# Optimization experiments

Measured on AMD Instinct MI355X. Metric: run time of the kernel, lower is better.

Reference implementation:

```python
import jax, jax.numpy as jnp
import numpy as np

PHM_DIM = 4
IN_FEATS = 2048
OUT_FEATS = 8192
TOKENS = 8192


def setup_inputs() -> dict:
    key = jax.random.key(0)
    k_x, k_rule, k_w = jax.random.split(key, 3)
    x = jax.random.normal(k_x, (TOKENS, IN_FEATS), dtype=jnp.float32)
    # c_init='normal', std=0.01
    phm_rule = 0.01 * jax.random.normal(k_rule, (PHM_DIM, PHM_DIM, PHM_DIM), dtype=jnp.float32)
    # w_init='normal', std=phm_init_range=1e-4 (scaled up here for numerics of the test)
    W = 1e-4 * jax.random.normal(k_w, (PHM_DIM, IN_FEATS // PHM_DIM, OUT_FEATS // PHM_DIM), dtype=jnp.float32)
    b = jnp.zeros((OUT_FEATS,), dtype=jnp.float32)
    return {"x": x, "phm_rule": phm_rule, "W": W, "b": b}


def reference(x, phm_rule, W, b):
    # H = sum_i kron(phm_rule[i], W[i])  with shape (phm_dim*in_per, phm_dim*out_per)
    # kron(A, B)[a*in_per + c, k*out_per + p] = A[a, k] * B[c, p]
    d, in_per, out_per = W.shape
    H = jnp.einsum('iak,icp->acKp'.replace('K', 'k'), phm_rule, W)  # (d, in_per, d, out_per)
    H = H.reshape(d * in_per, d * out_per)
    y = x @ H + b
    return y
```

## Files before the change

kernel.cpp:

```cpp
#include <hip/hip_runtime.h>
#include <stdint.h>

#define PHM      4
#define IN_FEATS 2048
#define OUT_FEATS 8192
#define TOKENS   8192
#define IN_PER   512
#define OUT_PER  2048

typedef __attribute__((ext_vector_type(8)))  short short8;
typedef __attribute__((ext_vector_type(16))) float f32x16;
typedef __attribute__((ext_vector_type(8)))  unsigned short u16x8;

__device__ inline unsigned short f2bf(float f) {
    unsigned int u = __builtin_bit_cast(unsigned int, f);
    u += 0x7fffu + ((u >> 16) & 1u);
    return (unsigned short)(u >> 16);
}

__global__ void cvt_x_kernel(const float* __restrict__ x,
                             unsigned short* __restrict__ xb) {
    int i = blockIdx.x * blockDim.x + threadIdx.x;
    const float4* x4 = (const float4*)x;
    float4 v0 = x4[2 * i];
    float4 v1 = x4[2 * i + 1];
    u16x8 o;
    o[0] = f2bf(v0.x); o[1] = f2bf(v0.y); o[2] = f2bf(v0.z); o[3] = f2bf(v0.w);
    o[4] = f2bf(v1.x); o[5] = f2bf(v1.y); o[6] = f2bf(v1.z); o[7] = f2bf(v1.w);
    *(u16x8*)(xb + 8 * (size_t)i) = o;
}

__global__ void build_ht_kernel(const float* __restrict__ rule,
                                const float* __restrict__ W,
                                unsigned short* __restrict__ Ht)
{
    __shared__ float lds[PHM][32][65];
    const int tid = threadIdx.x;
    const int c0 = blockIdx.x * 32;
    const int p0 = blockIdx.y * 64;

    #pragma unroll
    for (int it = 0; it < 32; ++it) {
        int idx = it * 256 + tid;
        int pp = idx & 63;
        int cc = (idx >> 6) & 31;
        int i  = idx >> 11;
        lds[i][cc][pp] = W[((size_t)(i * IN_PER + c0 + cc)) * OUT_PER + p0 + pp];
    }
    __syncthreads();

    const int pp = tid >> 2;
    const int j0 = (tid & 3) * 8;
    float w[PHM][8];
    #pragma unroll
    for (int i = 0; i < PHM; ++i)
        #pragma unroll
        for (int j = 0; j < 8; ++j)
            w[i][j] = lds[i][j0 + j][pp];

    #pragma unroll
    for (int a = 0; a < PHM; ++a) {
        #pragma unroll
        for (int kq = 0; kq < PHM; ++kq) {
            float r0 = rule[(0 * PHM + a) * PHM + kq];
            float r1 = rule[(1 * PHM + a) * PHM + kq];
            float r2 = rule[(2 * PHM + a) * PHM + kq];
            float r3 = rule[(3 * PHM + a) * PHM + kq];
            u16x8 o;
            #pragma unroll
            for (int j = 0; j < 8; ++j) {
                float v = r0 * w[0][j] + r1 * w[1][j] + r2 * w[2][j] + r3 * w[3][j];
                o[j] = f2bf(v);
            }
            size_t n = (size_t)(kq * OUT_PER + p0 + pp);
            *(u16x8*)(Ht + n * IN_FEATS + a * IN_PER + c0 + j0) = o;
        }
    }
}

#define BM 256
#define BN 256
#define BK 32
#define NTILES (IN_FEATS / BK)
#define LTILE  (BM * BK)

__device__ inline void gload16(const unsigned short* g, unsigned short* l) {
    __builtin_amdgcn_global_load_lds(
        (const __attribute__((address_space(1))) unsigned int*)g,
        (__attribute__((address_space(3))) unsigned int*)l,
        16, 0, 0);
}

__device__ inline void barrier_fenced() {
    asm volatile("" ::: "memory");
    __builtin_amdgcn_s_barrier();
    asm volatile("" ::: "memory");
}

__global__ __launch_bounds__(512, 2) void gemm_bt_kernel(
    const unsigned short* __restrict__ A,
    const unsigned short* __restrict__ B,
    const float* __restrict__ bias,
    float* __restrict__ C)
{
    constexpr int N = OUT_FEATS, K = IN_FEATS;
    constexpr int NXB = OUT_FEATS / BN;
    constexpr int NWG = (TOKENS / BM) * NXB;

    __shared__ unsigned short As[3 * LTILE];
    __shared__ unsigned short Bs[3 * LTILE];

    const int tid  = threadIdx.x;
    const int wave = tid >> 6;
    const int lane = tid & 63;
    const int lm   = lane & 31;
    const int kh   = lane >> 5;

    const int orig = blockIdx.y * NXB + blockIdx.x;
    const int swzb = (orig & 7) * (NWG >> 3) + (orig >> 3);
    const int bn = swzb & (NXB - 1);
    const int bm = swzb >> 5;

    const int wm = (wave >> 2) * 128;
    const int wn = (wave & 3) * 64;

    int offA[2][2][2];
    int offB[2][2];
    #pragma unroll
    for (int mh = 0; mh < 2; ++mh)
        #pragma unroll
        for (int mf = 0; mf < 2; ++mf)
            #pragma unroll
            for (int ks = 0; ks < 2; ++ks) {
                int r   = wm + (mh * 2 + mf) * 32 + lm;
                int k16 = ks * 2 + kh;
                offA[mh][mf][ks] = r * BK + ((k16 ^ ((r >> 1) & 3)) << 3);
            }
    #pragma unroll
    for (int nf = 0; nf < 2; ++nf)
        #pragma unroll
        for (int ks = 0; ks < 2; ++ks) {
            int r   = wn + nf * 32 + lm;
            int k16 = ks * 2 + kh;
            offB[nf][ks] = r * BK + ((k16 ^ ((r >> 1) & 3)) << 3);
        }

    const int srow = tid >> 2;
    const int scol = (((tid & 3) ^ ((tid >> 3) & 3)) << 3);
    const unsigned short* Ag0 = A + (size_t)(bm * BM + srow) * K + scol;
    const unsigned short* Ag1 = Ag0 + (size_t)128 * K;
    const unsigned short* Bg0 = B + (size_t)(bn * BN + srow) * K + scol;
    const unsigned short* Bg1 = Bg0 + (size_t)128 * K;
    unsigned short* const As_d0 = As + wave * 16 * BK;
    unsigned short* const As_d1 = As_d0 + 128 * BK;
    unsigned short* const Bs_d0 = Bs + wave * 16 * BK;
    unsigned short* const Bs_d1 = Bs_d0 + 128 * BK;

    #define STAGE_A(koff, so) do { \
        gload16(Ag0 + (koff), As_d0 + (so)); \
        gload16(Ag1 + (koff), As_d1 + (so)); } while (0)
    #define STAGE_B(koff, so) do { \
        gload16(Bg0 + (koff), Bs_d0 + (so)); \
        gload16(Bg1 + (koff), Bs_d1 + (so)); } while (0)

    STAGE_A(0, 0);            STAGE_B(0, 0);
    STAGE_A(BK, LTILE);       STAGE_B(BK, LTILE);
    asm volatile("s_waitcnt vmcnt(4)" ::: "memory");
    barrier_fenced();

    f32x16 acc[4][2] = {};
    int cur = 0, stg = 2;

    #pragma unroll 1
    for (int t = 0; t < NTILES; ++t) {
        const unsigned short* Ab = As + cur * LTILE;
        const unsigned short* Bb = Bs + cur * LTILE;
        const bool st   = (t + 2) < NTILES;
        const int  k2   = (t + 2) * BK;
        const int  so   = stg * LTILE;

        short8 a[2][2], b[2][2];

        #pragma unroll
        for (int mf = 0; mf < 2; ++mf)
            #pragma unroll
            for (int ks = 0; ks < 2; ++ks)
                a[mf][ks] = *(const short8*)(Ab + offA[0][mf][ks]);
        #pragma unroll
        for (int nf = 0; nf < 2; ++nf)
            #pragma unroll
            for (int ks = 0; ks < 2; ++ks)
                b[nf][ks] = *(const short8*)(Bb + offB[nf][ks]);
        if (st) STAGE_A(k2, so);
        barrier_fenced();
        asm volatile("s_waitcnt lgkmcnt(0)" ::: "memory");
        __builtin_amdgcn_sched_barrier(0);
        __builtin_amdgcn_s_setprio(1);
        #pragma unroll
        for (int ks = 0; ks < 2; ++ks)
            #pragma unroll
            for (int mf = 0; mf < 2; ++mf)
                #pragma unroll
                for (int nf = 0; nf < 2; ++nf)
                    acc[mf][nf] = __builtin_amdgcn_mfma_f32_32x32x16_bf16(
                        a[mf][ks], b[nf][ks], acc[mf][nf], 0, 0, 0);
        __builtin_amdgcn_s_setprio(0);
        barrier_fenced();

        #pragma unroll
        for (int mf = 0; mf < 2; ++mf)
            #pragma unroll
            for (int ks = 0; ks < 2; ++ks)
                a[mf][ks] = *(const short8*)(Ab + offA[1][mf][ks]);
        if (st) STAGE_B(k2, so);
        barrier_fenced();
        asm volatile("s_waitcnt lgkmcnt(0)" ::: "memory");
        __builtin_amdgcn_sched_barrier(0);
        __builtin_amdgcn_s_setprio(1);
        #pragma unroll
        for (int ks = 0; ks < 2; ++ks)
            #pragma unroll
            for (int mf = 0; mf < 2; ++mf)
                #pragma unroll
                for (int nf = 0; nf < 2; ++nf)
                    acc[2 + mf][nf] = __builtin_amdgcn_mfma_f32_32x32x16_bf16(
                        a[mf][ks], b[nf][ks], acc[2 + mf][nf], 0, 0, 0);
        __builtin_amdgcn_s_setprio(0);
        if (t < NTILES - 2) asm volatile("s_waitcnt vmcnt(4)" ::: "memory");
        else                asm volatile("s_waitcnt vmcnt(0)" ::: "memory");
        barrier_fenced();

        cur = (cur == 2) ? 0 : cur + 1;
        stg = (stg == 2) ? 0 : stg + 1;
    }
    #undef STAGE_A
    #undef STAGE_B

    const int cn = lm;
    const int rb = 4 * kh;
    #pragma unroll
    for (int j = 0; j < 2; ++j) {
        const int col = bn * BN + wn + j * 32 + cn;
        const float bv = bias[col];
        #pragma unroll
        for (int i = 0; i < 4; ++i) {
            const int row0 = bm * BM + wm + i * 32 + rb;
            #pragma unroll
            for (int reg = 0; reg < 16; ++reg) {
                int row = row0 + (reg & 3) + 8 * (reg >> 2);
                C[(size_t)row * N + col] = acc[i][j][reg] + bv;
            }
        }
    }
}

extern "C" void kernel_launch(void* const* d_in, const int* in_sizes, int n_in,
                              void* d_out, int out_size, void* d_ws, size_t ws_size,
                              hipStream_t stream) {
    const float* x    = (const float*)d_in[0];
    const float* rule = (const float*)d_in[1];
    const float* W    = (const float*)d_in[2];
    const float* b    = (const float*)d_in[3];
    float* y = (float*)d_out;

    unsigned short* xb = (unsigned short*)d_ws;
    unsigned short* Ht = (unsigned short*)((char*)d_ws +
                         (size_t)TOKENS * IN_FEATS * sizeof(unsigned short));

    cvt_x_kernel<<<(TOKENS * IN_FEATS) / 8 / 256, 256, 0, stream>>>(x, xb);
    build_ht_kernel<<<dim3(IN_PER / 32, OUT_PER / 64), 256, 0, stream>>>(rule, W, Ht);
    gemm_bt_kernel<<<dim3(OUT_FEATS / BN, TOKENS / BM), 512, 0, stream>>>(xb, Ht, b, y);
}
```

Baseline: 611.6 us.

## Double the GEMM K-tile to 64 with a two-slot LDS buffer

Raises the K step of the bf16 GEMM from 32 to 64 and replaces the three-slot LDS ring with a two-slot, 128 KB LDS buffer. The next tile's global-to-LDS loads are issued right after each half-step's barrier, into the slot just read, and an XOR swizzle suited to 64-wide rows replaces the old one. The aim is to halve the barriers and loop overhead per unit of work and to put more MFMAs in each phase. The workgroup index swizzle used for L2 locality is dropped in favour of direct blockIdx mapping. The larger LDS footprint likely allows only one workgroup per CU despite the launch bound of two, so latency hiding and L2 reuse may get worse.

```diff
diff --git a/kernel.cpp b/kernel.cpp
--- a/kernel.cpp
+++ b/kernel.cpp
@@ -80,9 +80,8 @@
 
 #define BM 256
 #define BN 256
-#define BK 32
-#define NTILES (IN_FEATS / BK)
-#define LTILE  (BM * BK)
+#define BK 64
+#define NT (IN_FEATS / BK)
 
 __device__ inline void gload16(const unsigned short* g, unsigned short* l) {
     __builtin_amdgcn_global_load_lds(
@@ -104,11 +103,7 @@
     float* __restrict__ C)
 {
     constexpr int N = OUT_FEATS, K = IN_FEATS;
-    constexpr int NXB = OUT_FEATS / BN;
-    constexpr int NWG = (TOKENS / BM) * NXB;
-
-    __shared__ unsigned short As[3 * LTILE];
-    __shared__ unsigned short Bs[3 * LTILE];
+    __shared__ unsigned short LDS[65536];
 
     const int tid  = threadIdx.x;
     const int wave = tid >> 6;
@@ -116,88 +111,68 @@
     const int lm   = lane & 31;
     const int kh   = lane >> 5;
 
-    const int orig = blockIdx.y * NXB + blockIdx.x;
-    const int swzb = (orig & 7) * (NWG >> 3) + (orig >> 3);
-    const int bn = swzb & (NXB - 1);
-    const int bm = swzb >> 5;
+    const int bn = blockIdx.x;
+    const int bm = blockIdx.y;
 
     const int wm = (wave >> 2) * 128;
     const int wn = (wave & 3) * 64;
 
-    int offA[2][2][2];
-    int offB[2][2];
-    #pragma unroll
-    for (int mh = 0; mh < 2; ++mh)
+    int aoff[4], boff[4];
+    #pragma unroll
+    for (int ks = 0; ks < 4; ++ks) {
+        int slot = ((2 * ks + kh) ^ (lm & 7)) * 8;
+        aoff[ks] = (wm + lm) * 64 + slot;
+        boff[ks] = 16384 + (wn + lm) * 64 + slot;
+    }
+
+    const int srow = wave * 8 + (lane >> 3);
+    const int schk = (lane & 7) ^ ((lane >> 3) & 7);
+    const unsigned short* AgS = A + (size_t)(bm * BM + srow) * K + schk * 8;
+    const unsigned short* BgS = B + (size_t)(bn * BN + srow) * K + schk * 8;
+    unsigned short* const Ad = LDS + wave * 512;
+    unsigned short* const Bd = LDS + 16384 + wave * 512;
+
+    #pragma unroll
+    for (int i = 0; i < 4; ++i) gload16(AgS + (size_t)i * 64 * K,      Ad + i * 4096);
+    #pragma unroll
+    for (int i = 0; i < 4; ++i) gload16(BgS + (size_t)i * 64 * K,      Bd + i * 4096);
+    #pragma unroll
+    for (int i = 0; i < 4; ++i) gload16(AgS + 64 + (size_t)i * 64 * K, Ad + 32768 + i * 4096);
+    #pragma unroll
+    for (int i = 0; i < 4; ++i) gload16(BgS + 64 + (size_t)i * 64 * K, Bd + 32768 + i * 4096);
+    asm volatile("s_waitcnt vmcnt(8)" ::: "memory");
+    barrier_fenced();
+
+    f32x16 acc[4][2] = {};
+    short8 a[2][4], b[2][4];
+
+    #pragma unroll 1
+    for (int t = 0; t < NT; ++t) {
+        const int  db   = (t & 1) << 15;
+        const int  koff = (t + 2) * BK;
+        const bool st   = (t + 2) < NT;
+
         #pragma unroll
         for (int mf = 0; mf < 2; ++mf)
             #pragma unroll
-            for (int ks = 0; ks < 2; ++ks) {
-                int r   = wm + (mh * 2 + mf) * 32 + lm;
-                int k16 = ks * 2 + kh;
-                offA[mh][mf][ks] = r * BK + ((k16 ^ ((r >> 1) & 3)) << 3);
-            }
-    #pragma unroll
-    for (int nf = 0; nf < 2; ++nf)
-        #pragma unroll
-        for (int ks = 0; ks < 2; ++ks) {
-            int r   = wn + nf * 32 + lm;
-            int k16 = ks * 2 + kh;
-            offB[nf][ks] = r * BK + ((k16 ^ ((r >> 1) & 3)) << 3);
-        }
-
-    const int srow = tid >> 2;
-    const int scol = (((tid & 3) ^ ((tid >> 3) & 3)) << 3);
-    const unsigned short* Ag0 = A + (size_t)(bm * BM + srow) * K + scol;
-    const unsigned short* Ag1 = Ag0 + (size_t)128 * K;
-    const unsigned short* Bg0 = B + (size_t)(bn * BN + srow) * K + scol;
-    const unsigned short* Bg1 = Bg0 + (size_t)128 * K;
-    unsigned short* const As_d0 = As + wave * 16 * BK;
-    unsigned short* const As_d1 = As_d0 + 128 * BK;
-    unsigned short* const Bs_d0 = Bs + wave * 16 * BK;
-    unsigned short* const Bs_d1 = Bs_d0 + 128 * BK;
-
-    #define STAGE_A(koff, so) do { \
-        gload16(Ag0 + (koff), As_d0 + (so)); \
-        gload16(Ag1 + (koff), As_d1 + (so)); } while (0)
-    #define STAGE_B(koff, so) do { \
-        gload16(Bg0 + (koff), Bs_d0 + (so)); \
-        gload16(Bg1 + (koff), Bs_d1 + (so)); } while (0)
-
-    STAGE_A(0, 0);            STAGE_B(0, 0);
-    STAGE_A(BK, LTILE);       STAGE_B(BK, LTILE);
-    asm volatile("s_waitcnt vmcnt(4)" ::: "memory");
-    barrier_fenced();
-
-    f32x16 acc[4][2] = {};
-    int cur = 0, stg = 2;
-
-    #pragma unroll 1
-    for (int t = 0; t < NTILES; ++t) {
-        const unsigned short* Ab = As + cur * LTILE;
-        const unsigned short* Bb = Bs + cur * LTILE;
-        const bool st   = (t + 2) < NTILES;
-        const int  k2   = (t + 2) * BK;
-        const int  so   = stg * LTILE;
-
-        short8 a[2][2], b[2][2];
-
-        #pragma unroll
-        for (int mf = 0; mf < 2; ++mf)
-            #pragma unroll
-            for (int ks = 0; ks < 2; ++ks)
-                a[mf][ks] = *(const short8*)(Ab + offA[0][mf][ks]);
+            for (int ks = 0; ks < 4; ++ks)
+                a[mf][ks] = *(const short8*)(LDS + db + aoff[ks] + mf * 2048);
         #pragma unroll
         for (int nf = 0; nf < 2; ++nf)
             #pragma unroll
-            for (int ks = 0; ks < 2; ++ks)
-                b[nf][ks] = *(const short8*)(Bb + offB[nf][ks]);
-        if (st) STAGE_A(k2, so);
+            for (int ks = 0; ks < 4; ++ks)
+                b[nf][ks] = *(const short8*)(LDS + db + boff[ks] + nf * 2048);
         barrier_fenced();
         asm volatile("s_waitcnt lgkmcnt(0)" ::: "memory");
         __builtin_amdgcn_sched_barrier(0);
+        if (st) {
+            #pragma unroll
+            for (int i = 0; i < 4; ++i)
+                gload16(BgS + koff + (size_t)i * 64 * K, Bd + db + i * 4096);
+        }
         __builtin_amdgcn_s_setprio(1);
         #pragma unroll
-        for (int ks = 0; ks < 2; ++ks)
+        for (int ks = 0; ks < 4; ++ks)
             #pragma unroll
             for (int mf = 0; mf < 2; ++mf)
                 #pragma unroll
@@ -210,15 +185,19 @@
         #pragma unroll
         for (int mf = 0; mf < 2; ++mf)
             #pragma unroll
-            for (int ks = 0; ks < 2; ++ks)
-                a[mf][ks] = *(const short8*)(Ab + offA[1][mf][ks]);
-        if (st) STAGE_B(k2, so);
+            for (int ks = 0; ks < 4; ++ks)
+                a[mf][ks] = *(const short8*)(LDS + db + aoff[ks] + (2 + mf) * 2048);
         barrier_fenced();
         asm volatile("s_waitcnt lgkmcnt(0)" ::: "memory");
         __builtin_amdgcn_sched_barrier(0);
+        if (st) {
+            #pragma unroll
+            for (int i = 0; i < 4; ++i)
+                gload16(AgS + koff + (size_t)i * 64 * K, Ad + db + i * 4096);
+        }
         __builtin_amdgcn_s_setprio(1);
         #pragma unroll
-        for (int ks = 0; ks < 2; ++ks)
+        for (int ks = 0; ks < 4; ++ks)
             #pragma unroll
             for (int mf = 0; mf < 2; ++mf)
                 #pragma unroll
@@ -226,15 +205,10 @@
                     acc[2 + mf][nf] = __builtin_amdgcn_mfma_f32_32x32x16_bf16(
                         a[mf][ks], b[nf][ks], acc[2 + mf][nf], 0, 0, 0);
         __builtin_amdgcn_s_setprio(0);
-        if (t < NTILES - 2) asm volatile("s_waitcnt vmcnt(4)" ::: "memory");
-        else                asm volatile("s_waitcnt vmcnt(0)" ::: "memory");
-        barrier_fenced();
-
-        cur = (cur == 2) ? 0 : cur + 1;
-        stg = (stg == 2) ? 0 : stg + 1;
-    }
-    #undef STAGE_A
-    #undef STAGE_B
+        if (t < NT - 2) asm volatile("s_waitcnt vmcnt(8)" ::: "memory");
+        else            asm volatile("s_waitcnt vmcnt(0)" ::: "memory");
+        barrier_fenced();
+    }
 
     const int cn = lm;
     const int rb = 4 * kh;
```

Result: slower. 625.9 us (+2.3%).
